# Optimization experiments

Measured on AMD Instinct MI355X. Metric: run time of the kernel, lower is better.

The kernel has to match this reference:

```python
import jax, jax.numpy as jnp
import numpy as np

TEMP = 0.07
EPS = 1e-8
NUM_CLASSES = 7
THRESH = 0.3


def setup_inputs() -> dict:
    key = jax.random.key(0)
    k1, k2, k3, k4, k5 = jax.random.split(key, 5)
    N, H, E, C = 8192, 128, 256, NUM_CLASSES
    reps = jax.random.normal(k1, (N, H), dtype=jnp.float32)
    labels = jax.random.randint(k2, (N,), 0, C, dtype=jnp.int64 if jax.config.jax_enable_x64 else jnp.int32)
    centers = jax.random.normal(k3, (C, E), dtype=jnp.float32)
    fc_w = jax.random.normal(k4, (H, E), dtype=jnp.float32) * (1.0 / np.sqrt(E))
    fc_b = jax.random.normal(k5, (H,), dtype=jnp.float32) * 0.01
    return {"reps": reps, "labels": labels, "centers": centers, "fc_w": fc_w, "fc_b": fc_b}


def reference(reps, labels, centers, fc_w, fc_b):
    # fc(default_centers): [C, H]
    curr_centers = centers @ fc_w.T + fc_b
    pad_labels = jnp.arange(NUM_CLASSES, dtype=labels.dtype)

    all_reps = jnp.concatenate([reps, curr_centers], axis=0)      # [M, H]
    all_labels = jnp.concatenate([labels, pad_labels], axis=0)    # [M]
    B = reps.shape[0]
    M = all_reps.shape[0]

    # cosine similarity via normalized matmul (avoids [B,M,H] broadcast)
    norms = jnp.sqrt(jnp.sum(all_reps * all_reps, axis=-1))
    rn = all_reps / jnp.maximum(norms, 1e-8)[:, None]
    cos = rn[:B] @ rn.T                                           # [B, M]

    scores = (1.0 + cos) * 0.5 + EPS
    eye = (jnp.arange(B)[:, None] == jnp.arange(M)[None, :]).astype(scores.dtype)
    scores = scores * (1.0 - eye) / TEMP
    # torch uses .item() on the max -> a non-differentiable constant
    scores = scores - jax.lax.stop_gradient(jnp.max(scores))
    e = jnp.exp(scores)

    pos_mask = (labels[:, None] == all_labels[None, :]).astype(scores.dtype)  # [B, M]
    mask = 1.0 - eye

    pos_sum = jnp.sum(e * pos_mask * mask, axis=-1)
    neg_sum = jnp.sum(e * (1.0 - pos_mask), axis=-1)
    probs = pos_sum / (pos_sum + neg_sum)
    probs = probs / (jnp.sum(pos_mask * mask, axis=-1) + EPS)

    loss_vec = -jnp.log(probs + EPS)
    loss_mask = (loss_vec > THRESH).astype(loss_vec.dtype)
    denom = jax.lax.stop_gradient(jnp.sum(loss_mask)) + EPS
    loss = jnp.sum(loss_vec * loss_mask) / denom
    return loss
```

## Files before the change

### kernel.cpp

```cpp
#include <hip/hip_runtime.h>
#include <hip/hip_bf16.h>

#define BN 8192
#define MM 8199
#define MP 8208
#define HH 128
#define EE 256
#define GX2 64
#define GY 16
#define NUM_HIST 7

typedef __attribute__((ext_vector_type(8))) short short8;
typedef __attribute__((ext_vector_type(4))) float floatx4;


__global__ __launch_bounds__(256)
void prep_kernel(const float* __restrict__ reps,
                 const int* __restrict__ labels,
                 const float* __restrict__ centers,
                 const float* __restrict__ fc_w,
                 const float* __restrict__ fc_b,
                 __hip_bfloat16* __restrict__ rnt,
                 int* __restrict__ labp,
                 float* __restrict__ tot) {
  const int wid = threadIdx.x >> 6, lane = threadIdx.x & 63;
  const int b = blockIdx.x;
  if (b < 2048) {
    if (threadIdx.x < 8) tot[b * 8 + threadIdx.x] = 0.f;
    const int r = b * 4 + wid;
    float2 v = ((const float2*)(reps + (size_t)r * HH))[lane];
    float ss = v.x * v.x + v.y * v.y;
#pragma unroll
    for (int m = 1; m < 64; m <<= 1) ss += __shfl_xor(ss, m);
    float inv = 1.0f / fmaxf(sqrtf(ss), 1e-8f);
    __hip_bfloat162 h2;
    h2.x = __float2bfloat16(v.x * inv);
    h2.y = __float2bfloat16(v.y * inv);
    size_t o = (size_t)(r >> 4) * 1024 + (lane >> 2) * 64 + (r & 15) * 4 + (lane & 3);
    ((__hip_bfloat162*)rnt)[o] = h2;
    if (lane == 0) labp[r] = labels[r];
  } else {
    __shared__ float currs[7 * HH];
    for (int o = threadIdx.x; o < 7 * HH; o += 256) {
      int c = o >> 7, h = o & 127;
      const float4* ce = (const float4*)(centers + c * EE);
      const float4* w  = (const float4*)(fc_w + h * EE);
      float s = 0.f;
#pragma unroll 4
      for (int j = 0; j < EE / 4; ++j) {
        float4 a = ce[j], bb = w[j];
        s += a.x * bb.x + a.y * bb.y + a.z * bb.z + a.w * bb.w;
      }
      currs[o] = s + fc_b[h];
    }
    __syncthreads();
    for (int k = 0; k < 4; ++k) {
      int c = wid * 4 + k;
      int r = BN + c;
      float2 v = make_float2(0.f, 0.f);
      if (c < 7) v = ((const float2*)(currs + c * HH))[lane];
      float ss = v.x * v.x + v.y * v.y;
#pragma unroll
      for (int m = 1; m < 64; m <<= 1) ss += __shfl_xor(ss, m);
      float inv = 1.0f / fmaxf(sqrtf(ss), 1e-8f);
      __hip_bfloat162 h2;
      h2.x = __float2bfloat16(v.x * inv);
      h2.y = __float2bfloat16(v.y * inv);
      size_t o = (size_t)(r >> 4) * 1024 + (lane >> 2) * 64 + (r & 15) * 4 + (lane & 3);
      ((__hip_bfloat162*)rnt)[o] = h2;
      if (lane == 0) labp[r] = (r < MM) ? r - BN : -1;
    }
  }
}

__global__ __launch_bounds__(256, 2)
void main_kernel(const __hip_bfloat16* __restrict__ rnt,
                 const int* __restrict__ labp,
                 float* __restrict__ tot,
                 float* __restrict__ pos) {
  __shared__ short lbuf[2][8192];
  const int lane = threadIdx.x & 63;
  const int w    = threadIdx.x >> 6;
  const int q = lane >> 4, col = lane & 15;
  const int ibase = blockIdx.x * 128;
  const short* rns = (const short*)rnt;

  short8 afrag[2][4];
  int tix[2];
#pragma unroll
  for (int it = 0; it < 2; ++it) {
    tix[it] = blockIdx.x * 8 + w * 2 + it;
    const short* base = rns + (size_t)tix[it] * 2048 + lane * 8;
    afrag[it][0] = *(const short8*)(base);
    afrag[it][1] = *(const short8*)(base + 512);
    afrag[it][2] = *(const short8*)(base + 1024);
    afrag[it][3] = *(const short8*)(base + 1536);
  }
  int labi[2][4];
#pragma unroll
  for (int it = 0; it < 2; ++it)
#pragma unroll
    for (int r = 0; r < 4; ++r)
      labi[it][r] = labp[ibase + (w * 2 + it) * 16 + q * 4 + r];

  float stot[2][4] = {};
  float spos[2][4] = {};
  const float K2 = 10.30496147f;

  auto accum = [&](short8 b0, short8 b1, short8 b2, short8 b3, int t, int labj) {
#pragma unroll
    for (int it = 0; it < 2; ++it) {
      floatx4 acc = {0.f, 0.f, 0.f, 0.f};
      acc = __builtin_amdgcn_mfma_f32_16x16x32_bf16(afrag[it][0], b0, acc, 0, 0, 0);
      acc = __builtin_amdgcn_mfma_f32_16x16x32_bf16(afrag[it][1], b1, acc, 0, 0, 0);
      acc = __builtin_amdgcn_mfma_f32_16x16x32_bf16(afrag[it][2], b2, acc, 0, 0, 0);
      acc = __builtin_amdgcn_mfma_f32_16x16x32_bf16(afrag[it][3], b3, acc, 0, 0, 0);
      float ev[4];
#pragma unroll
      for (int r = 0; r < 4; ++r) {
        float e = __builtin_amdgcn_exp2f(fmaf(acc[r], K2, -K2));
        ev[r] = e;
        stot[it][r] += e;
        spos[it][r] += (labj == labi[it][r]) ? e : 0.f;
      }
      if (t == tix[it]) {
#pragma unroll
        for (int r = 0; r < 4; ++r)
          if (col == q * 4 + r) { stot[it][r] -= ev[r]; spos[it][r] -= ev[r]; }
      }
    }
  };

  auto stage_quad = [&](int buf, int t) {
    const short* g = rns + (size_t)t * 2048 + threadIdx.x * 8;
#pragma unroll
    for (int k = 0; k < 4; ++k)
      __builtin_amdgcn_global_load_lds(
          (const __attribute__((address_space(1))) void*)(g + k * 2048),
          (__attribute__((address_space(3))) void*)&lbuf[buf][threadIdx.x * 8 + k * 2048],
          16, 0, 0);
  };

  const int t0 = blockIdx.y * 32;

  stage_quad(0, t0);
  __syncthreads();

  for (int p = 0; p < 8; ++p) {
    const int cur = p & 1;
    const int t = t0 + p * 4;
    if (p < 7) stage_quad(cur ^ 1, t + 4);

    int labj[4];
#pragma unroll
    for (int u = 0; u < 4; ++u) labj[u] = labp[(t + u) * 16 + col];

    const short* lb = &lbuf[cur][0];
#pragma unroll
    for (int u = 0; u < 4; ++u) {
      const short* s = lb + u * 2048;
      short8 b0 = *(const short8*)(s + lane * 8);
      short8 b1 = *(const short8*)(s + 512 + lane * 8);
      short8 b2 = *(const short8*)(s + 1024 + lane * 8);
      short8 b3 = *(const short8*)(s + 1536 + lane * 8);
      accum(b0, b1, b2, b3, t + u, labj[u]);
    }
    __syncthreads();
  }

  if (blockIdx.y == GY - 1) {
    const short* g = rns + (size_t)512 * 2048 + lane * 8;
    short8 b0 = *(const short8*)(g);
    short8 b1 = *(const short8*)(g + 512);
    short8 b2 = *(const short8*)(g + 1024);
    short8 b3 = *(const short8*)(g + 1536);
    accum(b0, b1, b2, b3, 512, labp[512 * 16 + col]);
  }

#pragma unroll
  for (int it = 0; it < 2; ++it)
#pragma unroll
    for (int r = 0; r < 4; ++r) {
      float tt = stot[it][r], pp = spos[it][r];
#pragma unroll
      for (int m = 1; m <= 8; m <<= 1) {
        tt += __shfl_xor(tt, m);
        pp += __shfl_xor(pp, m);
      }
      if (col == 0) {
        int i = ibase + (w * 2 + it) * 16 + q * 4 + r;
        atomicAdd(&tot[i], tt);
        atomicAdd(&pos[i], pp);
      }
    }
}

__global__ __launch_bounds__(1024)
void loss_kernel(const float* __restrict__ tot,
                 const float* __restrict__ pos,
                 const int* __restrict__ labels,
                 float* __restrict__ out) {
  __shared__ int hist[NUM_HIST];
  __shared__ float s1[16], s2[16];
  const int tid = threadIdx.x;
  const int lane = tid & 63, wid = tid >> 6;
  if (tid < NUM_HIST) hist[tid] = 0;
  __syncthreads();
  int c0 = 0, c1 = 0, c2 = 0, c3 = 0, c4 = 0, c5 = 0, c6 = 0;
  for (int i = tid; i < BN; i += 1024) {
    int lab = labels[i];
    unsigned long long m0 = __ballot(lab == 0);
    unsigned long long m1 = __ballot(lab == 1);
    unsigned long long m2 = __ballot(lab == 2);
    unsigned long long m3 = __ballot(lab == 3);
    unsigned long long m4 = __ballot(lab == 4);
    unsigned long long m5 = __ballot(lab == 5);
    unsigned long long m6 = __ballot(lab == 6);
    if (lane == 0) {
      c0 += __popcll(m0); c1 += __popcll(m1); c2 += __popcll(m2);
      c3 += __popcll(m3); c4 += __popcll(m4); c5 += __popcll(m5);
      c6 += __popcll(m6);
    }
  }
  if (lane == 0) {
    atomicAdd(&hist[0], c0); atomicAdd(&hist[1], c1); atomicAdd(&hist[2], c2);
    atomicAdd(&hist[3], c3); atomicAdd(&hist[4], c4); atomicAdd(&hist[5], c5);
    atomicAdd(&hist[6], c6);
  }
  __syncthreads();
  const float K2 = 10.30496147f;
  const float epad9 = 9.0f * exp2f(-K2);
  float lsum = 0.f, msum = 0.f;
  for (int i = tid; i < BN; i += 1024) {
    float t = tot[i] - epad9;
    float p = pos[i];
    float c = (float)hist[labels[i]];
    float pr = (p / t) / (c + 1e-8f);
    float lv = -logf(pr + 1e-8f);
    if (lv > 0.3f) { lsum += lv; msum += 1.f; }
  }
#pragma unroll
  for (int m = 1; m < 64; m <<= 1) {
    lsum += __shfl_xor(lsum, m);
    msum += __shfl_xor(msum, m);
  }
  if (lane == 0) { s1[wid] = lsum; s2[wid] = msum; }
  __syncthreads();
  if (wid == 0) {
    float a = (lane < 16) ? s1[lane] : 0.f;
    float b = (lane < 16) ? s2[lane] : 0.f;
#pragma unroll
    for (int m = 1; m < 16; m <<= 1) {
      a += __shfl_xor(a, m);
      b += __shfl_xor(b, m);
    }
    if (lane == 0) out[0] = a / (b + 1e-8f);
  }
}

extern "C" void kernel_launch(void* const* d_in, const int* in_sizes, int n_in,
                              void* d_out, int out_size, void* d_ws, size_t ws_size,
                              hipStream_t stream) {
  const float* reps    = (const float*)d_in[0];
  const int*   labels  = (const int*)d_in[1];
  const float* centers = (const float*)d_in[2];
  const float* fc_w    = (const float*)d_in[3];
  const float* fc_b    = (const float*)d_in[4];
  float* out = (float*)d_out;

  char* ws = (char*)d_ws;
  int* labp   = (int*)(ws + 4096);
  __hip_bfloat16* rnt = (__hip_bfloat16*)(ws + 40960);
  float* tot = (float*)(ws + 40960 + 2101248);
  float* pos = tot + BN;

  prep_kernel<<<2049, 256, 0, stream>>>(reps, labels, centers, fc_w, fc_b, rnt, labp, tot);
  main_kernel<<<dim3(GX2, GY), 256, 0, stream>>>(rnt, labp, tot, pos);
  loss_kernel<<<1, 1024, 0, stream>>>(tot, pos, labels, out);
}
```

Measured before the change: 131.2 us.

## Deepen LDS prefetch to a 4-buffer ring with explicit vmcnt waits

The two-stage LDS double buffer becomes a four-buffer ring that keeps three quads of B tiles in flight through global_load_lds. Each phase waits with an explicit s_waitcnt vmcnt count and a single barrier, instead of a full __syncthreads after every quad. All 32 column labels are loaded into registers up front, so per-phase label loads no longer sit in the loop. The aim is to hide global-load latency behind the MFMA and exp work. In exchange, LDS use per block doubles and register pressure rises, which could hurt occupancy at two blocks per CU.

```diff
diff --git a/kernel.cpp b/kernel.cpp
--- a/kernel.cpp
+++ b/kernel.cpp
@@ -78,7 +78,7 @@
                  const int* __restrict__ labp,
                  float* __restrict__ tot,
                  float* __restrict__ pos) {
-  __shared__ short lbuf[2][8192];
+  __shared__ short lbuf[4][8192];
   const int lane = threadIdx.x & 63;
   const int w    = threadIdx.x >> 6;
   const int q = lane >> 4, col = lane & 15;
@@ -103,6 +103,12 @@
     for (int r = 0; r < 4; ++r)
       labi[it][r] = labp[ibase + (w * 2 + it) * 16 + q * 4 + r];
 
+  const int t0 = blockIdx.y * 32;
+
+  int labjall[32];
+#pragma unroll
+  for (int s = 0; s < 32; ++s) labjall[s] = labp[(t0 + s) * 16 + col];
+
   float stot[2][4] = {};
   float spos[2][4] = {};
   const float K2 = 10.30496147f;
@@ -141,21 +147,8 @@
           16, 0, 0);
   };
 
-  const int t0 = blockIdx.y * 32;
-
-  stage_quad(0, t0);
-  __syncthreads();
-
-  for (int p = 0; p < 8; ++p) {
-    const int cur = p & 1;
-    const int t = t0 + p * 4;
-    if (p < 7) stage_quad(cur ^ 1, t + 4);
-
-    int labj[4];
-#pragma unroll
-    for (int u = 0; u < 4; ++u) labj[u] = labp[(t + u) * 16 + col];
-
-    const short* lb = &lbuf[cur][0];
+  auto compute_quad = [&](int buf, int t, int sp) {
+    const short* lb = &lbuf[buf][0];
 #pragma unroll
     for (int u = 0; u < 4; ++u) {
       const short* s = lb + u * 2048;
@@ -163,10 +156,33 @@
       short8 b1 = *(const short8*)(s + 512 + lane * 8);
       short8 b2 = *(const short8*)(s + 1024 + lane * 8);
       short8 b3 = *(const short8*)(s + 1536 + lane * 8);
-      accum(b0, b1, b2, b3, t + u, labj[u]);
-    }
-    __syncthreads();
-  }
+      accum(b0, b1, b2, b3, t + u, labjall[sp * 4 + u]);
+    }
+  };
+
+  stage_quad(0, t0);
+  stage_quad(1, t0 + 4);
+  stage_quad(2, t0 + 8);
+
+#define PHASE(P, VN)                                                    \
+  {                                                                     \
+    asm volatile("s_waitcnt vmcnt(" #VN ")" ::: "memory");              \
+    __builtin_amdgcn_sched_barrier(0);                                  \
+    __builtin_amdgcn_s_barrier();                                       \
+    __builtin_amdgcn_sched_barrier(0);                                  \
+    if ((P) < 5) stage_quad(((P) + 3) & 3, t0 + ((P) + 3) * 4);         \
+    compute_quad((P) & 3, t0 + (P) * 4, (P));                           \
+  }
+
+  PHASE(0, 8)
+  PHASE(1, 8)
+  PHASE(2, 8)
+  PHASE(3, 8)
+  PHASE(4, 8)
+  PHASE(5, 8)
+  PHASE(6, 4)
+  PHASE(7, 0)
+#undef PHASE
 
   if (blockIdx.y == GY - 1) {
     const short* g = rns + (size_t)512 * 2048 + lane * 8;
```

Result: slower. 133.8 us (+2.0%).
